# Kernel optimization log

Hardware: AMD Instinct MI355X
Metric: run time of the kernel (lower is better)

Reference implementation:

```python
import jax, jax.numpy as jnp
import numpy as np
from jax import lax

N_CHANNELS = 64
N_FILTERS = 256
N_LAYERS = 9  # residual blocks use dilations 2**1 .. 2**(N_LAYERS-1)


def causal_conv1d(x, w, dilation):
    """Causal dilated conv. x: [B,T,Cin], w: [K,Cin,Cout]."""
    pad = (w.shape[0] - 1) * dilation
    return lax.conv_general_dilated(
        x, w, window_strides=(1,), padding=[(pad, 0)],
        rhs_dilation=(dilation,), dimension_numbers=("NWC", "WIO", "NWC"))


def setup_inputs() -> dict:
    key = jax.random.key(0)
    ks = jax.random.split(key, 12)
    B, T, C, F, L = 8, 4096, N_CHANNELS, N_FILTERS, N_LAYERS
    s = lambda fan_in: 1.0 / np.sqrt(fan_in)
    return {
        "x": jax.random.normal(ks[0], (B, T, C), jnp.float32),
        "Wc": jax.random.normal(ks[1], (2, C, F), jnp.float32) * s(2 * C),
        "Wf": jax.random.normal(ks[2], (L - 1, 2, F, F), jnp.float32) * s(2 * F),
        "Wg": jax.random.normal(ks[3], (L - 1, 2, F, F), jnp.float32) * s(2 * F),
        "Wr": jax.random.normal(ks[4], (L - 1, F, F), jnp.float32) * s(F),
        "br": jnp.zeros((L - 1, F), jnp.float32),
        "Ws": jax.random.normal(ks[5], (L - 1, F, F), jnp.float32) * s(F),
        "bs": jnp.zeros((L - 1, F), jnp.float32),
        "Wd1": jax.random.normal(ks[6], (F, C), jnp.float32) * s(F),
        "bd1": jnp.zeros((C,), jnp.float32),
        "Wd2": jax.random.normal(ks[7], (C, C), jnp.float32) * s(C),
        "bd2": jnp.zeros((C,), jnp.float32),
    }


def reference(x, Wc, Wf, Wg, Wr, br, Ws, bs, Wd1, bd1, Wd2, bd2):
    # Initial causal conv, dilation 1, no bias.
    out = causal_conv1d(x, Wc, 1)  # [B,T,F]
    skip_sum = jnp.zeros_like(out)
    for i in range(N_LAYERS - 1):
        d = 2 ** (i + 1)
        f = causal_conv1d(out, Wf[i], d)
        g = causal_conv1d(out, Wg[i], d)
        z = jnp.tanh(f) * jax.nn.sigmoid(g)
        out = out + jnp.einsum("btf,fo->bto", z, Wr[i]) + br[i]
        skip_sum = skip_sum + jnp.einsum("btf,fo->bto", z, Ws[i]) + bs[i]
    h = jax.nn.selu(skip_sum)
    h = jnp.einsum("btf,fc->btc", h, Wd1) + bd1
    h = jax.nn.selu(h)
    h = jnp.einsum("btc,co->bto", h, Wd2) + bd2
    return h
```

## Files before the change

### kernel.cpp

```cpp
#include <hip/hip_runtime.h>
#include <cstdint>

typedef unsigned short u16;
typedef unsigned int u32;
typedef __attribute__((ext_vector_type(8))) short s8v;
typedef __attribute__((ext_vector_type(4))) float f4v;

#define FCH 256

__device__ __forceinline__ float bf2f(u16 u){ return __uint_as_float(((u32)u)<<16); }
__device__ __forceinline__ u16 f2bf(float x){
  u32 u = __float_as_uint(x);
  u += 0x7fffu + ((u>>16)&1u);
  return (u16)(u>>16);
}
__device__ __forceinline__ uint4 pack8(float4 a, float4 b){
  uint4 o;
  o.x = (u32)f2bf(a.x) | ((u32)f2bf(a.y)<<16);
  o.y = (u32)f2bf(a.z) | ((u32)f2bf(a.w)<<16);
  o.z = (u32)f2bf(b.x) | ((u32)f2bf(b.y)<<16);
  o.w = (u32)f2bf(b.z) | ((u32)f2bf(b.w)<<16);
  return o;
}
__device__ __forceinline__ float seluf(float x){
  const float sc = 1.0507009873554805f, al = 1.6732632423543772f;
  return x > 0.f ? sc*x : sc*al*(__expf(x)-1.f);
}
__device__ __forceinline__ s8v ldmask(const u16* p, u32 m){
  uint4 r = *reinterpret_cast<const uint4*>(p);
  r.x &= m; r.y &= m; r.z &= m; r.w &= m;
  s8v v; *reinterpret_cast<uint4*>(&v) = r;
  return v;
}
__device__ __forceinline__ int xcd_tile(int bid, int nT8){
  return nT8 ? ((bid & 7) * nT8 + (bid >> 3)) : bid;
}

__global__ __launch_bounds__(256) void pack_kernel(
    const float* __restrict__ Wc, const float* __restrict__ Wf, const float* __restrict__ Wg,
    const float* __restrict__ Wr, const float* __restrict__ Ws,
    const float* __restrict__ Wd1, const float* __restrict__ Wd2,
    u16* __restrict__ Bp1, u16* __restrict__ Bp2, u16* __restrict__ Bp0,
    u16* __restrict__ BpD1, u16* __restrict__ BpD2)
{
  int gid = blockIdx.x*256 + threadIdx.x;
  int frag = gid >> 6;
  int lane = gid & 63;
  int q = lane >> 4, i15 = lane & 15;
  u16 v[8];
  u16* dst;
  if (frag < 4096) {
    int layer = frag >> 9, rem = frag & 511;
    int kc = rem >> 5, nt = rem & 31;
    int n = nt*16 + i15;
    const float* W = (n < 256) ? Wf : Wg;
    int nn = (n < 256) ? n : n - 256;
    #pragma unroll
    for (int j = 0; j < 8; ++j) {
      int k = kc*32 + q*8 + j;
      int tap = k >> 8, cin = k & 255;
      v[j] = f2bf(W[((size_t)((layer*2 + tap)*256 + cin))*256 + nn]);
    }
    dst = Bp1 + (size_t)frag*512 + lane*8;
  } else if (frag < 6144) {
    int f = frag - 4096;
    int layer = f >> 8, rem = f & 255;
    int kc = rem >> 5, nt = rem & 31;
    int n = nt*16 + i15;
    const float* W = (n < 256) ? Wr : Ws;
    int nn = (n < 256) ? n : n - 256;
    #pragma unroll
    for (int j = 0; j < 8; ++j) {
      int k = kc*32 + q*8 + j;
      v[j] = f2bf(W[((size_t)(layer*256 + k))*256 + nn]);
    }
    dst = Bp2 + (size_t)f*512 + lane*8;
  } else if (frag < 6208) {
    int f = frag - 6144;
    int kc = f >> 4, nt = f & 15;
    int n = nt*16 + i15;
    #pragma unroll
    for (int j = 0; j < 8; ++j) {
      int k = kc*32 + q*8 + j;
      int tap = k >> 6, cin = k & 63;
      v[j] = f2bf(Wc[(size_t)(tap*64 + cin)*256 + n]);
    }
    dst = Bp0 + (size_t)f*512 + lane*8;
  } else if (frag < 6240) {
    int f = frag - 6208;
    int kc = f >> 2, nt = f & 3;
    int n = nt*16 + i15;
    #pragma unroll
    for (int j = 0; j < 8; ++j) {
      int k = kc*32 + q*8 + j;
      v[j] = f2bf(Wd1[(size_t)k*64 + n]);
    }
    dst = BpD1 + (size_t)f*512 + lane*8;
  } else if (frag < 6248) {
    int f = frag - 6240;
    int kc = f >> 2, nt = f & 3;
    int n = nt*16 + i15;
    #pragma unroll
    for (int j = 0; j < 8; ++j) {
      int k = kc*32 + q*8 + j;
      v[j] = f2bf(Wd2[(size_t)k*64 + n]);
    }
    dst = BpD2 + (size_t)f*512 + lane*8;
  } else return;
  uint4 o;
  o.x = (u32)v[0] | ((u32)v[1] << 16);
  o.y = (u32)v[2] | ((u32)v[3] << 16);
  o.z = (u32)v[4] | ((u32)v[5] << 16);
  o.w = (u32)v[6] | ((u32)v[7] << 16);
  *reinterpret_cast<uint4*>(dst) = o;
}

__global__ __launch_bounds__(256, 2) void conv0_kernel(
    const float* __restrict__ x, u16* __restrict__ outBf,
    const u16* __restrict__ Bp0, int nT8)
{
  __shared__ __align__(16) u16 ldsA[2][2048];
  const int tid = threadIdx.x;
  const int w = tid >> 6, lane = tid & 63, q = lane >> 4, i15 = lane & 15;
  const int rb = xcd_tile(blockIdx.x, nT8) * 64;
  const int sm = tid >> 2, sg = tid & 3;
  const int grow = rb + sm;
  const int tpos = grow & 4095;
  const int sunit = ((sm >> 4)*64 + sg*16 + ((sm & 15) ^ (sg << 1))) * 8;
  const int runit = (q*16 + (i15 ^ (q << 1))) * 8;

  f4v acc[4][4];
  #pragma unroll
  for (int jj = 0; jj < 4; ++jj)
    #pragma unroll
    for (int mt = 0; mt < 4; ++mt)
      acc[jj][mt] = (f4v){0.f,0.f,0.f,0.f};

  float4 f0 = {0.f,0.f,0.f,0.f}, f1 = {0.f,0.f,0.f,0.f};
  if (tpos >= 1) {
    const float* px = x + (size_t)(grow-1)*64 + sg*8;
    f0 = *reinterpret_cast<const float4*>(px);
    f1 = *reinterpret_cast<const float4*>(px + 4);
  }
  *reinterpret_cast<uint4*>(&ldsA[0][sunit]) = pack8(f0, f1);
  s8v bcur[4], bnxt[4];
  #pragma unroll
  for (int jj = 0; jj < 4; ++jj)
    bcur[jj] = *reinterpret_cast<const s8v*>(Bp0 + ((size_t)(w + 4*jj)*64 + lane)*8);
  __syncthreads();

  for (int kc = 0; kc < 4; ++kc) {
    const int cur = kc & 1;
    uint4 an = {0u,0u,0u,0u};
    if (kc < 3) {
      int kg = (kc+1)*32 + sg*8;
      int tap = kg >> 6, col = kg & 63;
      float4 g0 = {0.f,0.f,0.f,0.f}, g1 = {0.f,0.f,0.f,0.f};
      if (tap) {
        const float* px = x + (size_t)grow*64 + col;
        g0 = *reinterpret_cast<const float4*>(px);
        g1 = *reinterpret_cast<const float4*>(px + 4);
      } else if (tpos >= 1) {
        const float* px = x + (size_t)(grow-1)*64 + col;
        g0 = *reinterpret_cast<const float4*>(px);
        g1 = *reinterpret_cast<const float4*>(px + 4);
      }
      an = pack8(g0, g1);
      #pragma unroll
      for (int jj = 0; jj < 4; ++jj)
        bnxt[jj] = *reinterpret_cast<const s8v*>(Bp0 + (((size_t)(kc+1)*16 + (w + 4*jj))*64 + lane)*8);
    }
    s8v af[4];
    #pragma unroll
    for (int mt = 0; mt < 4; ++mt)
      af[mt] = *reinterpret_cast<const s8v*>(&ldsA[cur][mt*512 + runit]);
    #pragma unroll
    for (int jj = 0; jj < 4; ++jj)
      #pragma unroll
      for (int mt = 0; mt < 4; ++mt)
        acc[jj][mt] = __builtin_amdgcn_mfma_f32_16x16x32_bf16(af[mt], bcur[jj], acc[jj][mt], 0,0,0);
    if (kc < 3) {
      *reinterpret_cast<uint4*>(&ldsA[cur ^ 1][sunit]) = an;
      #pragma unroll
      for (int jj = 0; jj < 4; ++jj) bcur[jj] = bnxt[jj];
    }
    __syncthreads();
  }

  #pragma unroll
  for (int jj = 0; jj < 4; ++jj) {
    const int cc = (w + 4*jj)*16 + i15;
    #pragma unroll
    for (int mt = 0; mt < 4; ++mt)
      #pragma unroll
      for (int r = 0; r < 4; ++r) {
        const int g2 = rb + mt*16 + q*4 + r;
        outBf[(size_t)g2*FCH + cc] = f2bf(acc[jj][mt][r]);
      }
  }
}

__global__ __launch_bounds__(256, 3) void layer_kernel(
    const u16* __restrict__ inBf, u16* __restrict__ outBf,
    u16* __restrict__ skipB,
    const u16* __restrict__ Bp1, const u16* __restrict__ Bp2,
    const float* __restrict__ br, const float* __restrict__ bs,
    int dil, int first, int nT8)
{
  __shared__ __align__(16) u16 ldsZ[32*264];
  const int tid = threadIdx.x;
  const int w = tid >> 6, lane = tid & 63, q = lane >> 4, i15 = lane & 15;
  const int rb = xcd_tile(blockIdx.x, nT8) * 32;

  f4v acc[8][2];
  #pragma unroll
  for (int jj = 0; jj < 8; ++jj)
    #pragma unroll
    for (int mt = 0; mt < 2; ++mt)
      acc[jj][mt] = (f4v){0.f,0.f,0.f,0.f};

  {
    const u16* a0p[2];
    const u16* a1p[2];
    u32 am[2];
    #pragma unroll
    for (int mt = 0; mt < 2; ++mt) {
      const int row = rb + mt*16 + i15;
      const bool v = (row & 4095) >= dil;
      a0p[mt] = inBf + (size_t)(v ? row - dil : row)*FCH + q*8;
      a1p[mt] = inBf + (size_t)row*FCH + q*8;
      am[mt]  = v ? 0xffffffffu : 0u;
    }

    s8v bcur[8], bnxt[8], afc[2], afn[2];
    #pragma unroll
    for (int jj = 0; jj < 8; ++jj)
      bcur[jj] = *reinterpret_cast<const s8v*>(Bp1 + ((size_t)(w + 4*jj)*64 + lane)*8);
    #pragma unroll
    for (int mt = 0; mt < 2; ++mt)
      afc[mt] = ldmask(a0p[mt], am[mt]);

    #pragma unroll 2
    for (int kc = 0; kc < 16; ++kc) {
      const int kn = kc + 1;
      if (kn < 16) {
        #pragma unroll
        for (int jj = 0; jj < 8; ++jj)
          bnxt[jj] = *reinterpret_cast<const s8v*>(Bp1 + (((size_t)kn*32 + (w + 4*jj))*64 + lane)*8);
        if (kn < 8) {
          #pragma unroll
          for (int mt = 0; mt < 2; ++mt)
            afn[mt] = ldmask(a0p[mt] + kn*32, am[mt]);
        } else {
          #pragma unroll
          for (int mt = 0; mt < 2; ++mt)
            afn[mt] = *reinterpret_cast<const s8v*>(a1p[mt] + (kn - 8)*32);
        }
      }
      #pragma unroll
      for (int jj = 0; jj < 8; ++jj)
        #pragma unroll
        for (int mt = 0; mt < 2; ++mt)
          acc[jj][mt] = __builtin_amdgcn_mfma_f32_16x16x32_bf16(afc[mt], bcur[jj], acc[jj][mt], 0,0,0);
      #pragma unroll
      for (int jj = 0; jj < 8; ++jj) bcur[jj] = bnxt[jj];
      afc[0] = afn[0]; afc[1] = afn[1];
    }
  }

  s8v b2c[8], b2n[8];
  #pragma unroll
  for (int jj = 0; jj < 8; ++jj)
    b2c[jj] = *reinterpret_cast<const s8v*>(Bp2 + ((size_t)(w + 4*jj)*64 + lane)*8);

  #pragma unroll
  for (int jj = 0; jj < 4; ++jj) {
    const int colb = (w + 4*jj)*16 + i15;
    #pragma unroll
    for (int mt = 0; mt < 2; ++mt)
      #pragma unroll
      for (int r = 0; r < 4; ++r) {
        float f = acc[jj][mt][r];
        float g = acc[jj+4][mt][r];
        float z = (1.f - 2.f/(__expf(2.f*f) + 1.f)) * (1.f/(1.f + __expf(-g)));
        ldsZ[(mt*16 + q*4 + r)*264 + colb] = f2bf(z);
      }
  }
  #pragma unroll
  for (int jj = 0; jj < 8; ++jj)
    #pragma unroll
    for (int mt = 0; mt < 2; ++mt)
      acc[jj][mt] = (f4v){0.f,0.f,0.f,0.f};
  __syncthreads();

  {
    s8v zfc[2], zfn[2];
    #pragma unroll
    for (int mt = 0; mt < 2; ++mt)
      zfc[mt] = *reinterpret_cast<const s8v*>(&ldsZ[(mt*16 + i15)*264 + q*8]);
    #pragma unroll 2
    for (int kc = 0; kc < 8; ++kc) {
      const int kn = kc + 1;
      if (kn < 8) {
        #pragma unroll
        for (int jj = 0; jj < 8; ++jj)
          b2n[jj] = *reinterpret_cast<const s8v*>(Bp2 + (((size_t)kn*32 + (w + 4*jj))*64 + lane)*8);
        #pragma unroll
        for (int mt = 0; mt < 2; ++mt)
          zfn[mt] = *reinterpret_cast<const s8v*>(&ldsZ[(mt*16 + i15)*264 + kn*32 + q*8]);
      }
      #pragma unroll
      for (int jj = 0; jj < 8; ++jj)
        #pragma unroll
        for (int mt = 0; mt < 2; ++mt)
          acc[jj][mt] = __builtin_amdgcn_mfma_f32_16x16x32_bf16(zfc[mt], b2c[jj], acc[jj][mt], 0,0,0);
      #pragma unroll
      for (int jj = 0; jj < 8; ++jj) b2c[jj] = b2n[jj];
      zfc[0] = zfn[0]; zfc[1] = zfn[1];
    }
  }

  u16 resv[4][2][4], skv[4][2][4];
  #pragma unroll
  for (int jj = 0; jj < 4; ++jj) {
    const int cc = (w + 4*jj)*16 + i15;
    #pragma unroll
    for (int mt = 0; mt < 2; ++mt)
      #pragma unroll
      for (int r = 0; r < 4; ++r)
        resv[jj][mt][r] = inBf[(size_t)(rb + mt*16 + q*4 + r)*FCH + cc];
  }
  if (!first) {
    #pragma unroll
    for (int jj = 0; jj < 4; ++jj) {
      const int cc = (w + 4*jj)*16 + i15;
      #pragma unroll
      for (int mt = 0; mt < 2; ++mt)
        #pragma unroll
        for (int r = 0; r < 4; ++r)
          skv[jj][mt][r] = skipB[(size_t)(rb + mt*16 + q*4 + r)*FCH + cc];
    }
  }
  #pragma unroll
  for (int jj = 0; jj < 8; ++jj) {
    const int nt = w + 4*jj;
    const bool isR = (jj < 4);
    const int cc = (isR ? nt*16 : (nt-16)*16) + i15;
    const float bias = isR ? br[cc] : bs[cc];
    #pragma unroll
    for (int mt = 0; mt < 2; ++mt)
      #pragma unroll
      for (int r = 0; r < 4; ++r) {
        const int g2 = rb + mt*16 + q*4 + r;
        float vv = acc[jj][mt][r] + bias;
        if (isR) vv += bf2f(resv[jj][mt][r]);
        else if (!first) vv += bf2f(skv[jj-4][mt][r]);
        u16 hv = f2bf(vv);
        if (isR) outBf[(size_t)g2*FCH + cc] = hv;
        else     skipB[(size_t)g2*FCH + cc] = hv;
      }
  }
}

__global__ __launch_bounds__(256, 2) void final_kernel(
    const u16* __restrict__ skipB, const u16* __restrict__ BpD1, const u16* __restrict__ BpD2,
    const float* __restrict__ bd1, const float* __restrict__ bd2, float* __restrict__ outp,
    int nT8)
{
  __shared__ __align__(16) u16 ldsH[64*264];
  __shared__ __align__(16) u16 ldsH2[64*72];
  const int tid = threadIdx.x;
  const int w = tid >> 6, lane = tid & 63, q = lane >> 4, i15 = lane & 15;
  const int rb = xcd_tile(blockIdx.x, nT8) * 64;
  const int sm = tid >> 2, sseg = tid & 3;

  {
    const u16* sp = skipB + (size_t)(rb + sm)*256 + sseg*64;
    u16* dr = &ldsH[sm*264 + sseg*64];
    #pragma unroll
    for (int u = 0; u < 8; ++u) {
      uint4 raw = *reinterpret_cast<const uint4*>(sp + u*8);
      u32 rr[4] = {raw.x, raw.y, raw.z, raw.w};
      uint4 o;
      u32 oo[4];
      #pragma unroll
      for (int p = 0; p < 4; ++p) {
        float e0 = seluf(bf2f((u16)(rr[p] & 0xffffu)));
        float e1 = seluf(bf2f((u16)(rr[p] >> 16)));
        oo[p] = (u32)f2bf(e0) | ((u32)f2bf(e1) << 16);
      }
      o.x = oo[0]; o.y = oo[1]; o.z = oo[2]; o.w = oo[3];
      *reinterpret_cast<uint4*>(dr + u*8) = o;
    }
  }
  __syncthreads();

  f4v a1[4];
  #pragma unroll
  for (int mt = 0; mt < 4; ++mt) a1[mt] = (f4v){0.f,0.f,0.f,0.f};
  for (int kc = 0; kc < 8; ++kc) {
    s8v b = *reinterpret_cast<const s8v*>(BpD1 + ((size_t)(kc*4 + w)*64 + lane)*8);
    #pragma unroll
    for (int mt = 0; mt < 4; ++mt) {
      s8v af = *reinterpret_cast<const s8v*>(&ldsH[(mt*16 + i15)*264 + kc*32 + q*8]);
      a1[mt] = __builtin_amdgcn_mfma_f32_16x16x32_bf16(af, b, a1[mt], 0,0,0);
    }
  }
  const float bb1 = bd1[w*16 + i15];
  #pragma unroll
  for (int mt = 0; mt < 4; ++mt)
    #pragma unroll
    for (int r = 0; r < 4; ++r)
      ldsH2[(mt*16 + q*4 + r)*72 + w*16 + i15] = f2bf(seluf(a1[mt][r] + bb1));
  __syncthreads();

  f4v a2[4];
  #pragma unroll
  for (int mt = 0; mt < 4; ++mt) a2[mt] = (f4v){0.f,0.f,0.f,0.f};
  #pragma unroll
  for (int kc = 0; kc < 2; ++kc) {
    s8v b = *reinterpret_cast<const s8v*>(BpD2 + ((size_t)(kc*4 + w)*64 + lane)*8);
    #pragma unroll
    for (int mt = 0; mt < 4; ++mt) {
      s8v af = *reinterpret_cast<const s8v*>(&ldsH2[(mt*16 + i15)*72 + kc*32 + q*8]);
      a2[mt] = __builtin_amdgcn_mfma_f32_16x16x32_bf16(af, b, a2[mt], 0,0,0);
    }
  }
  const float bb2 = bd2[w*16 + i15];
  #pragma unroll
  for (int mt = 0; mt < 4; ++mt)
    #pragma unroll
    for (int r = 0; r < 4; ++r)
      outp[(size_t)(rb + mt*16 + q*4 + r)*64 + w*16 + i15] = a2[mt][r] + bb2;
}

__global__ __launch_bounds__(256) void zero_kernel(uint4* __restrict__ outp, int n16)
{
  int i = blockIdx.x*256 + threadIdx.x;
  if (i < n16) outp[i] = (uint4){0u,0u,0u,0u};
}

extern "C" void kernel_launch(void* const* d_in, const int* in_sizes, int n_in,
                              void* d_out, int out_size, void* d_ws, size_t ws_size,
                              hipStream_t stream)
{
  (void)n_in;
  const float* x   = (const float*)d_in[0];
  const float* Wc  = (const float*)d_in[1];
  const float* Wf  = (const float*)d_in[2];
  const float* Wg  = (const float*)d_in[3];
  const float* Wr  = (const float*)d_in[4];
  const float* br  = (const float*)d_in[5];
  const float* Ws  = (const float*)d_in[6];
  const float* bs  = (const float*)d_in[7];
  const float* Wd1 = (const float*)d_in[8];
  const float* bd1 = (const float*)d_in[9];
  const float* Wd2 = (const float*)d_in[10];
  const float* bd2 = (const float*)d_in[11];

  const size_t ROWS = (size_t)in_sizes[0] / 64;
  const int gridC = (int)(ROWS / 64);
  const int gridL = (int)(ROWS / 32);
  const int nT8C = (gridC % 8 == 0) ? gridC / 8 : 0;
  const int nT8L = (gridL % 8 == 0) ? gridL / 8 : 0;

  const size_t packsB = (size_t)6248 * 512 * 2;
  const size_t bfBuf  = ROWS * 256 * 2;
  const size_t needB = packsB + 3*bfBuf;

  if (ws_size < needB) {
    int n16 = (out_size * 4) / 16;
    zero_kernel<<<(n16 + 255)/256, 256, 0, stream>>>((uint4*)d_out, n16);
    return;
  }

  char* ws = (char*)d_ws;
  u16* Bp1    = (u16*)ws;            ws += (size_t)4096*512*2;
  u16* Bp2    = (u16*)ws;            ws += (size_t)2048*512*2;
  u16* Bp0    = (u16*)ws;            ws += (size_t)64*512*2;
  u16* BpD1   = (u16*)ws;            ws += (size_t)32*512*2;
  u16* BpD2   = (u16*)ws;            ws += (size_t)8*512*2;
  u16* skipB  = (u16*)ws;            ws += bfBuf;
  u16* bufA   = (u16*)ws;            ws += bfBuf;
  u16* bufB   = (u16*)ws;            ws += bfBuf;

  pack_kernel<<<1562, 256, 0, stream>>>(Wc, Wf, Wg, Wr, Ws, Wd1, Wd2,
                                        Bp1, Bp2, Bp0, BpD1, BpD2);
  conv0_kernel<<<gridC, 256, 0, stream>>>(x, bufA, Bp0, nT8C);
  u16* bufs[2] = {bufA, bufB};
  for (int i = 0; i < 8; ++i) {
    layer_kernel<<<gridL, 256, 0, stream>>>(
        bufs[i & 1], bufs[(i + 1) & 1], skipB,
        Bp1 + (size_t)i*262144, Bp2 + (size_t)i*131072,
        br + i*256, bs + i*256, 2 << i, (i == 0) ? 1 : 0, nT8L);
  }
  final_kernel<<<gridC, 256, 0, stream>>>(skipB, BpD1, BpD2, bd1, bd2,
                                          (float*)d_out, nT8C);
}
```

Baseline: 542.6 us.

## Use 64-row tiles with 8 waves and triple-buffered weight prefetch in layer kernel

The layer kernel now processes 64 rows per block with 512 threads (8 waves), each wave computing 4 column tiles × 4 row tiles instead of 8 × 2. Each B-weight fragment loaded from global memory is therefore reused across more rows, halving weight traffic per output row. The k-loop is fully unrolled, with B operands prefetched two steps ahead through a 3-deep ring and A operands double-buffered. The grid halves and LDS doubles, which lowers occupancy and raises register pressure.

```diff
diff --git a/kernel.cpp b/kernel.cpp
--- a/kernel.cpp
+++ b/kernel.cpp
@@ -200,31 +200,31 @@
   }
 }
 
-__global__ __launch_bounds__(256, 3) void layer_kernel(
+__global__ __launch_bounds__(512, 2) void layer_kernel(
     const u16* __restrict__ inBf, u16* __restrict__ outBf,
     u16* __restrict__ skipB,
     const u16* __restrict__ Bp1, const u16* __restrict__ Bp2,
     const float* __restrict__ br, const float* __restrict__ bs,
     int dil, int first, int nT8)
 {
-  __shared__ __align__(16) u16 ldsZ[32*264];
+  __shared__ __align__(16) u16 ldsZ[64*264];
   const int tid = threadIdx.x;
   const int w = tid >> 6, lane = tid & 63, q = lane >> 4, i15 = lane & 15;
-  const int rb = xcd_tile(blockIdx.x, nT8) * 32;
-
-  f4v acc[8][2];
-  #pragma unroll
-  for (int jj = 0; jj < 8; ++jj)
-    #pragma unroll
-    for (int mt = 0; mt < 2; ++mt)
+  const int rb = xcd_tile(blockIdx.x, nT8) * 64;
+
+  f4v acc[4][4];
+  #pragma unroll
+  for (int jj = 0; jj < 4; ++jj)
+    #pragma unroll
+    for (int mt = 0; mt < 4; ++mt)
       acc[jj][mt] = (f4v){0.f,0.f,0.f,0.f};
 
   {
-    const u16* a0p[2];
-    const u16* a1p[2];
-    u32 am[2];
-    #pragma unroll
-    for (int mt = 0; mt < 2; ++mt) {
+    const u16* a0p[4];
+    const u16* a1p[4];
+    u32 am[4];
+    #pragma unroll
+    for (int mt = 0; mt < 4; ++mt) {
       const int row = rb + mt*16 + i15;
       const bool v = (row & 4095) >= dil;
       a0p[mt] = inBf + (size_t)(v ? row - dil : row)*FCH + q*8;
@@ -232,129 +232,132 @@
       am[mt]  = v ? 0xffffffffu : 0u;
     }
 
-    s8v bcur[8], bnxt[8], afc[2], afn[2];
-    #pragma unroll
-    for (int jj = 0; jj < 8; ++jj)
-      bcur[jj] = *reinterpret_cast<const s8v*>(Bp1 + ((size_t)(w + 4*jj)*64 + lane)*8);
-    #pragma unroll
-    for (int mt = 0; mt < 2; ++mt)
-      afc[mt] = ldmask(a0p[mt], am[mt]);
-
-    #pragma unroll 2
+    s8v bb[3][4], aa[2][4];
+    #pragma unroll
+    for (int jj = 0; jj < 4; ++jj) {
+      bb[0][jj] = *reinterpret_cast<const s8v*>(Bp1 + ((size_t)(w + 8*jj)*64 + lane)*8);
+      bb[1][jj] = *reinterpret_cast<const s8v*>(Bp1 + ((size_t)(32 + w + 8*jj)*64 + lane)*8);
+    }
+    #pragma unroll
+    for (int mt = 0; mt < 4; ++mt)
+      aa[0][mt] = ldmask(a0p[mt], am[mt]);
+
+    #pragma unroll
     for (int kc = 0; kc < 16; ++kc) {
-      const int kn = kc + 1;
-      if (kn < 16) {
+      if (kc + 2 < 16) {
+        const int kp = kc + 2;
         #pragma unroll
-        for (int jj = 0; jj < 8; ++jj)
-          bnxt[jj] = *reinterpret_cast<const s8v*>(Bp1 + (((size_t)kn*32 + (w + 4*jj))*64 + lane)*8);
+        for (int jj = 0; jj < 4; ++jj)
+          bb[kp % 3][jj] = *reinterpret_cast<const s8v*>(Bp1 + (((size_t)kp*32 + (w + 8*jj))*64 + lane)*8);
+      }
+      if (kc + 1 < 16) {
+        const int kn = kc + 1;
         if (kn < 8) {
           #pragma unroll
-          for (int mt = 0; mt < 2; ++mt)
-            afn[mt] = ldmask(a0p[mt] + kn*32, am[mt]);
+          for (int mt = 0; mt < 4; ++mt)
+            aa[kn & 1][mt] = ldmask(a0p[mt] + kn*32, am[mt]);
         } else {
           #pragma unroll
-          for (int mt = 0; mt < 2; ++mt)
-            afn[mt] = *reinterpret_cast<const s8v*>(a1p[mt] + (kn - 8)*32);
+          for (int mt = 0; mt < 4; ++mt)
+            aa[kn & 1][mt] = *reinterpret_cast<const s8v*>(a1p[mt] + (kn - 8)*32);
         }
       }
       #pragma unroll
-      for (int jj = 0; jj < 8; ++jj)
+      for (int jj = 0; jj < 4; ++jj)
         #pragma unroll
-        for (int mt = 0; mt < 2; ++mt)
-          acc[jj][mt] = __builtin_amdgcn_mfma_f32_16x16x32_bf16(afc[mt], bcur[jj], acc[jj][mt], 0,0,0);
-      #pragma unroll
-      for (int jj = 0; jj < 8; ++jj) bcur[jj] = bnxt[jj];
-      afc[0] = afn[0]; afc[1] = afn[1];
-    }
-  }
-
-  s8v b2c[8], b2n[8];
-  #pragma unroll
-  for (int jj = 0; jj < 8; ++jj)
-    b2c[jj] = *reinterpret_cast<const s8v*>(Bp2 + ((size_t)(w + 4*jj)*64 + lane)*8);
-
+        for (int mt = 0; mt < 4; ++mt)
+          acc[jj][mt] = __builtin_amdgcn_mfma_f32_16x16x32_bf16(aa[kc & 1][mt], bb[kc % 3][jj], acc[jj][mt], 0,0,0);
+    }
+  }
+
+  s8v s2b[3][4];
   #pragma unroll
   for (int jj = 0; jj < 4; ++jj) {
-    const int colb = (w + 4*jj)*16 + i15;
-    #pragma unroll
-    for (int mt = 0; mt < 2; ++mt)
+    s2b[0][jj] = *reinterpret_cast<const s8v*>(Bp2 + ((size_t)(w + 8*jj)*64 + lane)*8);
+    s2b[1][jj] = *reinterpret_cast<const s8v*>(Bp2 + ((size_t)(32 + w + 8*jj)*64 + lane)*8);
+  }
+
+  #pragma unroll
+  for (int jj = 0; jj < 2; ++jj) {
+    const int colb = (w + 8*jj)*16 + i15;
+    #pragma unroll
+    for (int mt = 0; mt < 4; ++mt)
       #pragma unroll
       for (int r = 0; r < 4; ++r) {
         float f = acc[jj][mt][r];
-        float g = acc[jj+4][mt][r];
+        float g = acc[jj+2][mt][r];
         float z = (1.f - 2.f/(__expf(2.f*f) + 1.f)) * (1.f/(1.f + __expf(-g)));
         ldsZ[(mt*16 + q*4 + r)*264 + colb] = f2bf(z);
       }
   }
   #pragma unroll
-  for (int jj = 0; jj < 8; ++jj)
-    #pragma unroll
-    for (int mt = 0; mt < 2; ++mt)
+  for (int jj = 0; jj < 4; ++jj)
+    #pragma unroll
+    for (int mt = 0; mt < 4; ++mt)
       acc[jj][mt] = (f4v){0.f,0.f,0.f,0.f};
   __syncthreads();
 
   {
-    s8v zfc[2], zfn[2];
-    #pragma unroll
-    for (int mt = 0; mt < 2; ++mt)
-      zfc[mt] = *reinterpret_cast<const s8v*>(&ldsZ[(mt*16 + i15)*264 + q*8]);
-    #pragma unroll 2
+    s8v s2a[2][4];
+    #pragma unroll
+    for (int mt = 0; mt < 4; ++mt)
+      s2a[0][mt] = *reinterpret_cast<const s8v*>(&ldsZ[(mt*16 + i15)*264 + q*8]);
+    #pragma unroll
     for (int kc = 0; kc < 8; ++kc) {
-      const int kn = kc + 1;
-      if (kn < 8) {
+      if (kc + 2 < 8) {
+        const int kp = kc + 2;
         #pragma unroll
-        for (int jj = 0; jj < 8; ++jj)
-          b2n[jj] = *reinterpret_cast<const s8v*>(Bp2 + (((size_t)kn*32 + (w + 4*jj))*64 + lane)*8);
+        for (int jj = 0; jj < 4; ++jj)
+          s2b[kp % 3][jj] = *reinterpret_cast<const s8v*>(Bp2 + (((size_t)kp*32 + (w + 8*jj))*64 + lane)*8);
+      }
+      if (kc + 1 < 8) {
+        const int kn = kc + 1;
         #pragma unroll
-        for (int mt = 0; mt < 2; ++mt)
-          zfn[mt] = *reinterpret_cast<const s8v*>(&ldsZ[(mt*16 + i15)*264 + kn*32 + q*8]);
-      }
-      #pragma unroll
-      for (int jj = 0; jj < 8; ++jj)
+        for (int mt = 0; mt < 4; ++mt)
+          s2a[kn & 1][mt] = *reinterpret_cast<const s8v*>(&ldsZ[(mt*16 + i15)*264 + kn*32 + q*8]);
+      }
+      #pragma unroll
+      for (int jj = 0; jj < 4; ++jj)
         #pragma unroll
-        for (int mt = 0; mt < 2; ++mt)
-          acc[jj][mt] = __builtin_amdgcn_mfma_f32_16x16x32_bf16(zfc[mt], b2c[jj], acc[jj][mt], 0,0,0);
-      #pragma unroll
-      for (int jj = 0; jj < 8; ++jj) b2c[jj] = b2n[jj];
-      zfc[0] = zfn[0]; zfc[1] = zfn[1];
-    }
-  }
-
-  u16 resv[4][2][4], skv[4][2][4];
-  #pragma unroll
-  for (int jj = 0; jj < 4; ++jj) {
-    const int cc = (w + 4*jj)*16 + i15;
-    #pragma unroll
-    for (int mt = 0; mt < 2; ++mt)
+        for (int mt = 0; mt < 4; ++mt)
+          acc[jj][mt] = __builtin_amdgcn_mfma_f32_16x16x32_bf16(s2a[kc & 1][mt], s2b[kc % 3][jj], acc[jj][mt], 0,0,0);
+    }
+  }
+
+  u16 resv[2][4][4], skv[2][4][4];
+  #pragma unroll
+  for (int jj = 0; jj < 2; ++jj) {
+    const int cc = (w + 8*jj)*16 + i15;
+    #pragma unroll
+    for (int mt = 0; mt < 4; ++mt)
       #pragma unroll
       for (int r = 0; r < 4; ++r)
         resv[jj][mt][r] = inBf[(size_t)(rb + mt*16 + q*4 + r)*FCH + cc];
   }
   if (!first) {
     #pragma unroll
-    for (int jj = 0; jj < 4; ++jj) {
-      const int cc = (w + 4*jj)*16 + i15;
-      #pragma unroll
-      for (int mt = 0; mt < 2; ++mt)
+    for (int jj = 0; jj < 2; ++jj) {
+      const int cc = (w + 8*jj)*16 + i15;
+      #pragma unroll
+      for (int mt = 0; mt < 4; ++mt)
         #pragma unroll
         for (int r = 0; r < 4; ++r)
           skv[jj][mt][r] = skipB[(size_t)(rb + mt*16 + q*4 + r)*FCH + cc];
     }
   }
   #pragma unroll
-  for (int jj = 0; jj < 8; ++jj) {
-    const int nt = w + 4*jj;
-    const bool isR = (jj < 4);
-    const int cc = (isR ? nt*16 : (nt-16)*16) + i15;
+  for (int jj = 0; jj < 4; ++jj) {
+    const bool isR = (jj < 2);
+    const int cc = (w + 8*(isR ? jj : jj-2))*16 + i15;
     const float bias = isR ? br[cc] : bs[cc];
     #pragma unroll
-    for (int mt = 0; mt < 2; ++mt)
+    for (int mt = 0; mt < 4; ++mt)
       #pragma unroll
       for (int r = 0; r < 4; ++r) {
         const int g2 = rb + mt*16 + q*4 + r;
         float vv = acc[jj][mt][r] + bias;
         if (isR) vv += bf2f(resv[jj][mt][r]);
-        else if (!first) vv += bf2f(skv[jj-4][mt][r]);
+        else if (!first) vv += bf2f(skv[jj-2][mt][r]);
         u16 hv = f2bf(vv);
         if (isR) outBf[(size_t)g2*FCH + cc] = hv;
         else     skipB[(size_t)g2*FCH + cc] = hv;
@@ -460,9 +463,7 @@
 
   const size_t ROWS = (size_t)in_sizes[0] / 64;
   const int gridC = (int)(ROWS / 64);
-  const int gridL = (int)(ROWS / 32);
   const int nT8C = (gridC % 8 == 0) ? gridC / 8 : 0;
-  const int nT8L = (gridL % 8 == 0) ? gridL / 8 : 0;
 
   const size_t packsB = (size_t)6248 * 512 * 2;
   const size_t bfBuf  = ROWS * 256 * 2;
@@ -489,10 +490,10 @@
   conv0_kernel<<<gridC, 256, 0, stream>>>(x, bufA, Bp0, nT8C);
   u16* bufs[2] = {bufA, bufB};
   for (int i = 0; i < 8; ++i) {
-    layer_kernel<<<gridL, 256, 0, stream>>>(
+    layer_kernel<<<gridC, 512, 0, stream>>>(
         bufs[i & 1], bufs[(i + 1) & 1], skipB,
         Bp1 + (size_t)i*262144, Bp2 + (size_t)i*131072,
-        br + i*256, bs + i*256, 2 << i, (i == 0) ? 1 : 0, nT8L);
+        br + i*256, bs + i*256, 2 << i, (i == 0) ? 1 : 0, nT8C);
   }
   final_kernel<<<gridC, 256, 0, stream>>>(skipB, BpD1, BpD2, bd1, bd2,
                                           (float*)d_out, nT8C);
```

New measurement: 634.2 us. 1.17x slower.
